# Optimization experiments

Measured on AMD Instinct MI355X. Metric: run time of the kernel, lower is better.

Reference implementation:

```python
import math
import jax, jax.numpy as jnp
import numpy as np

B, S, D, H, KV = 2, 2048, 1024, 16, 4
HD = D // H  # 64
ROPE_BASE = 10000.0
RMS_EPS = 1.1920929e-07  # torch.finfo(float32).eps, F.rms_norm default


def setup_inputs() -> dict:
    key = jax.random.key(0)
    ks = jax.random.split(key, 5)
    x = jax.random.normal(ks[0], (B, S, D), jnp.float32)
    Wq = jax.random.normal(ks[1], (D, D), jnp.float32) * 0.02
    Wk = jax.random.normal(ks[2], (KV * HD, D), jnp.float32) * 0.02
    Wv = jax.random.normal(ks[3], (KV * HD, D), jnp.float32) * 0.02
    Wproj = jax.random.normal(ks[4], (D, D), jnp.float32) * 0.02
    q_gain = jnp.ones((H,), jnp.float32)  # qk_gain_init = 1.0
    return {"x": x, "Wq": Wq, "Wk": Wk, "Wv": Wv, "Wproj": Wproj, "q_gain": q_gain}


def _rms_norm(t):
    # F.rms_norm with no weight: t * rsqrt(mean(t^2) + eps)
    return t * jax.lax.rsqrt(jnp.mean(t * t, axis=-1, keepdims=True) + RMS_EPS)


def _rope(t, cos, sin):
    half = t.shape[-1] // 2
    t1, t2 = t[..., :half], t[..., half:]
    return jnp.concatenate([t1 * cos + t2 * sin, t1 * -sin + t2 * cos], axis=-1)


def reference(x, Wq, Wk, Wv, Wproj, q_gain):
    bsz, seqlen, dim = x.shape
    hd = dim // H
    # QKV projections (Linear weight layout [out, in])
    q = (x @ Wq.T).reshape(bsz, seqlen, H, hd).transpose(0, 2, 1, 3)    # [B,H,S,hd]
    k = (x @ Wk.T).reshape(bsz, seqlen, KV, hd).transpose(0, 2, 1, 3)   # [B,KV,S,hd]
    v = (x @ Wv.T).reshape(bsz, seqlen, KV, hd).transpose(0, 2, 1, 3)
    # per-head RMSNorm on q/k (no learned weight)
    q = _rms_norm(q)
    k = _rms_norm(k)
    # RoPE tables
    inv_freq = 1.0 / (ROPE_BASE ** (jnp.arange(0, hd, 2, dtype=jnp.float32) / hd))
    t = jnp.arange(seqlen, dtype=jnp.float32)
    freqs = t[:, None] * inv_freq[None, :]                              # [S, hd/2]
    cos = jnp.cos(freqs)[None, None]                                    # [1,1,S,hd/2]
    sin = jnp.sin(freqs)[None, None]
    q = _rope(q, cos, sin)
    k = _rope(k, cos, sin)
    # learned per-head query gain
    q = q * q_gain[None, :, None, None]
    # GQA: repeat_interleave kv heads to full head count
    rep = H // KV
    k = jnp.repeat(k, rep, axis=1)                                      # [B,H,S,hd]
    v = jnp.repeat(v, rep, axis=1)
    # causal SDPA, scale = 1/sqrt(head_dim)
    scores = jnp.einsum("bhqd,bhkd->bhqk", q, k) * (1.0 / math.sqrt(hd))
    causal = jnp.tril(jnp.ones((seqlen, seqlen), bool))
    scores = jnp.where(causal[None, None], scores, jnp.finfo(scores.dtype).min)
    attn = jax.nn.softmax(scores, axis=-1)
    y = jnp.einsum("bhqk,bhkd->bhqd", attn, v)
    y = y.transpose(0, 2, 1, 3).reshape(bsz, seqlen, dim)
    return y @ Wproj.T
```

## Files before the change

### kernel.cpp

```cpp
#include <hip/hip_runtime.h>

typedef unsigned short u16;
typedef __bf16 bf16_t;
typedef bf16_t bf16x8 __attribute__((ext_vector_type(8)));
typedef float f32x4 __attribute__((ext_vector_type(4)));
typedef u16 u16x8 __attribute__((ext_vector_type(8)));
typedef u16 u16x4 __attribute__((ext_vector_type(4)));

__device__ __forceinline__ u16 f2bf(float f) {
  unsigned u = __float_as_uint(f);
  u += 0x7fffu + ((u >> 16) & 1u);
  return (u16)(u >> 16);
}

__device__ __forceinline__ float bf2f(u16 u) {
  return __uint_as_float((unsigned)u << 16);
}

__device__ __forceinline__ unsigned cvtpk(float lo, float hi) {
  unsigned r;
  asm("v_cvt_pk_bf16_f32 %0, %1, %2" : "=v"(r) : "v"(lo), "v"(hi));
  return r;
}

__device__ __forceinline__ f32x4 mfma16(bf16x8 a, bf16x8 b, f32x4 c) {
  return __builtin_amdgcn_mfma_f32_16x16x32_bf16(a, b, c, 0, 0, 0);
}

__device__ __forceinline__ void gl2lds16(const u16* g, u16* l) {
  __builtin_amdgcn_global_load_lds(
      (__attribute__((address_space(1))) void*)(u16*)g,
      (__attribute__((address_space(3))) void*)l, 16, 0, 0);
}

__device__ __forceinline__ void cast8(const float* __restrict__ in,
                                      u16* __restrict__ out, int i) {
  float4 a = *(const float4*)&in[i];
  float4 b = *(const float4*)&in[i + 4];
  uint4 o;
  o.x = cvtpk(a.x, a.y);
  o.y = cvtpk(a.z, a.w);
  o.z = cvtpk(b.x, b.y);
  o.w = cvtpk(b.z, b.w);
  *(uint4*)&out[i] = o;
}

__global__ __launch_bounds__(256) void megacast(
    const float* __restrict__ x, const float* __restrict__ Wq,
    const float* __restrict__ Wk, const float* __restrict__ Wv,
    const float* __restrict__ Wp, u16* __restrict__ xb,
    u16* __restrict__ wallb, u16* __restrict__ wpb,
    float2* __restrict__ tbl) {
  const int blk = blockIdx.x;
  const int tid = threadIdx.x;
  if (blk < 2048) {
    cast8(x, xb, (blk * 256 + tid) * 8);
  } else if (blk < 2560) {
    cast8(Wq, wallb, ((blk - 2048) * 256 + tid) * 8);
  } else if (blk < 2688) {
    cast8(Wk, wallb + 1048576, ((blk - 2560) * 256 + tid) * 8);
  } else if (blk < 2816) {
    cast8(Wv, wallb + 1310720, ((blk - 2688) * 256 + tid) * 8);
  } else if (blk < 3328) {
    cast8(Wp, wpb, ((blk - 2816) * 256 + tid) * 8);
  } else {
    const int idx = (blk - 3328) * 256 + tid;
    const int s = idx >> 5, i = idx & 31;
    float inv = exp2f(-(float)i * (13.287712379549449f / 32.0f));
    float fr = (float)s * inv;
    float sn, cs;
    sincosf(fr, &sn, &cs);
    tbl[idx] = make_float2(cs, sn);
  }
}

template <int BM, int BN, bool O16>
__global__ __launch_bounds__(256) void gemm_bt(const u16* __restrict__ A,
                                               const u16* __restrict__ B,
                                               void* __restrict__ Cv,
                                               int M, int N, int K) {
  constexpr int FM = BM / 32;
  constexpr int FN = BN / 32;
  constexpr int NL = (BM + BN) / 32;
  __shared__ __align__(16) u16 As[2][BM][64];
  __shared__ __align__(16) u16 Bs[2][BN][64];
  const int tid = threadIdx.x;
  const int lane = tid & 63;
  const int lg = lane >> 4, li = lane & 15;
  const int wave = tid >> 6;
  const int wr = (wave >> 1) * (BM / 2), wc = (wave & 1) * (BN / 2);
  const int m0 = blockIdx.y * BM, n0 = blockIdx.x * BN;

  const int s_r = tid >> 3;
  const int s_c = (tid & 7) ^ ((tid >> 3) & 7);
  const int rdsw = li & 7;

  auto GSTAGE = [&](int buf, int k0) {
    const u16* ga = &A[(size_t)(m0 + s_r) * K + k0 + s_c * 8];
#pragma unroll
    for (int i = 0; i < BM / 32; i++)
      gl2lds16(ga + (size_t)(i * 32) * K, &As[buf][i * 32][0] + (size_t)tid * 8);
    const u16* gb = &B[(size_t)(n0 + s_r) * K + k0 + s_c * 8];
#pragma unroll
    for (int i = 0; i < BN / 32; i++)
      gl2lds16(gb + (size_t)(i * 32) * K, &Bs[buf][i * 32][0] + (size_t)tid * 8);
  };

  const f32x4 fz = {0.f, 0.f, 0.f, 0.f};
  f32x4 acc[FM][FN];
#pragma unroll
  for (int i = 0; i < FM; i++)
#pragma unroll
    for (int j = 0; j < FN; j++) acc[i][j] = fz;

  GSTAGE(0, 0);
  int buf = 0;
  const int nk = K >> 6;
  for (int t = 0; t < nk; ++t) {
    if (t + 1 < nk) {
      GSTAGE(buf ^ 1, (t + 1) * 64);
      if constexpr (NL == 6)
        asm volatile("s_waitcnt vmcnt(6)" ::: "memory");
      else if constexpr (NL == 7)
        asm volatile("s_waitcnt vmcnt(7)" ::: "memory");
      else
        asm volatile("s_waitcnt vmcnt(8)" ::: "memory");
    } else {
      asm volatile("s_waitcnt vmcnt(0)" ::: "memory");
    }
    __builtin_amdgcn_s_barrier();
#pragma unroll
    for (int kk = 0; kk < 2; kk++) {
      bf16x8 af[FM], bfr[FN];
#pragma unroll
      for (int i = 0; i < FM; i++)
        af[i] = *(const bf16x8*)&As[buf][wr + i * 16 + li]
                                   [((kk * 4 + lg) ^ rdsw) * 8];
#pragma unroll
      for (int j = 0; j < FN; j++)
        bfr[j] = *(const bf16x8*)&Bs[buf][wc + j * 16 + li]
                                    [((kk * 4 + lg) ^ rdsw) * 8];
      __builtin_amdgcn_s_setprio(1);
#pragma unroll
      for (int i = 0; i < FM; i++)
#pragma unroll
        for (int j = 0; j < FN; j++) acc[i][j] = mfma16(af[i], bfr[j], acc[i][j]);
      __builtin_amdgcn_s_setprio(0);
    }
    __builtin_amdgcn_s_barrier();
    buf ^= 1;
  }
#pragma unroll
  for (int i = 0; i < FM; i++)
#pragma unroll
    for (int j = 0; j < FN; j++)
#pragma unroll
      for (int r = 0; r < 4; r++) {
        const size_t idx =
            (size_t)(m0 + wr + i * 16 + lg * 4 + r) * N + n0 + wc + j * 16 + li;
        if constexpr (O16)
          ((u16*)Cv)[idx] = f2bf(acc[i][j][r]);
        else
          ((float*)Cv)[idx] = acc[i][j][r];
      }
}

__global__ __launch_bounds__(256) void rmsropeqk(const u16* __restrict__ in,
                                                 const float* __restrict__ qg,
                                                 u16* __restrict__ qhb,
                                                 u16* __restrict__ khb, int S,
                                                 const float2* __restrict__ tbl) {
  const int w = threadIdx.x >> 6;
  const int t = threadIdx.x & 63;
  const int row = blockIdx.x * 4 + w;
  const int h = blockIdx.y;
  const bool isq = h < 16;
  const int col = isq ? h * 64 : 1024 + (h - 16) * 64;
  const float v = bf2f(in[(size_t)row * 1536 + col + t]);
  float ss = v * v;
#pragma unroll
  for (int m = 1; m < 64; m <<= 1) ss += __shfl_xor(ss, m);
  const float vn = v * rsqrtf(ss * (1.0f / 64.0f) + 1.1920929e-07f);
  const float partner = __shfl_xor(vn, 32);
  const int b = row / S;
  const int s = row - b * S;
  const float2 cs2 = tbl[s * 32 + (t & 31)];
  float o = (t < 32) ? (vn * cs2.x + partner * cs2.y)
                     : (vn * cs2.x - partner * cs2.y);
  if (isq) {
    o *= 0.18033688011112042f * qg[h];
    qhb[((size_t)(b * 16 + h) * S + s) * 64 + t] = f2bf(o);
  } else {
    khb[((size_t)(b * 4 + (h - 16)) * S + s) * 64 + t] = f2bf(o);
  }
}

__global__ __launch_bounds__(256) void vcast2(const u16* __restrict__ qf,
                                              u16* __restrict__ vt, int S) {
  const int blk = blockIdx.x;
  const int sc = blk & 7;
  const int kv = (blk >> 3) & 3;
  const int b = blk >> 5;
  __shared__ u16 T[256][66];
  const int tid = threadIdx.x;
  const int dcol = tid & 63;
  const int w = tid >> 6;
  const u16* src =
      qf + (size_t)(b * S + sc * 256) * 1536 + 1280 + kv * 64 + dcol;
#pragma unroll 4
  for (int i = 0; i < 64; ++i) {
    const int sl = i * 4 + w;
    T[sl][dcol] = src[(size_t)sl * 1536];
  }
  __syncthreads();
  u16* dst = vt + (size_t)((b * 4 + kv) * 64) * S + sc * 256;
  const int l = tid & 63;
#pragma unroll 4
  for (int i = 0; i < 16; ++i) {
    const int drow = i * 4 + w;
    u16x4 v4;
    v4[0] = T[l * 4 + 0][drow];
    v4[1] = T[l * 4 + 1][drow];
    v4[2] = T[l * 4 + 2][drow];
    v4[3] = T[l * 4 + 3][drow];
    *(u16x4*)(dst + (size_t)drow * S + l * 4) = v4;
  }
}

__global__ __launch_bounds__(256) void attn8(const u16* __restrict__ qh,
                                             const u16* __restrict__ kh,
                                             const u16* __restrict__ vt,
                                             const float* __restrict__ qg,
                                             u16* __restrict__ y, int S) {
  const int bh = blockIdx.x & 31;
  const int g = blockIdx.x >> 5;
  const int d = g & 7, u = g >> 3;
  const int qb = (u == 0) ? 31 - d : (u == 1) ? 16 + d : (u == 2) ? 15 - d : d;
  const int h = bh & 15, b = bh >> 4;
  const int kvh = h >> 2;
  const int tid = threadIdx.x;
  const int wave = tid >> 6;
  const int lane = tid & 63;
  const int lg = lane >> 4, li = lane & 15;
  const int q0 = qb * 64 + wave * 16;
  const int qrow = q0 + li;
  const float mrow = 11.541560327111707f * fabsf(qg[h]);

  const u16* qp = qh + ((size_t)(b * 16 + h) * S + q0) * 64;
  const u16* kp = kh + (size_t)(b * 4 + kvh) * S * 64;
  const u16* vp = vt + (size_t)(b * 4 + kvh) * 64 * S;

  __shared__ __align__(16) u16 Ks[2][64][64];
  __shared__ __align__(16) u16 Vs[2][64][64];
  __shared__ __align__(16) u16 Ps[4][16][64];

  const int s_r0 = tid >> 3;
  const int s_c = (tid & 7) ^ ((tid >> 3) & 7);
  char* psrow = (char*)&Ps[wave][li][0];
  const int swz = li & 7;
  const int rdsw = li & 7;
  const f32x4 minit = {-mrow, -mrow, -mrow, -mrow};
  const f32x4 fz = {0.f, 0.f, 0.f, 0.f};
  const u16x8 ones_u = {0x3F80, 0x3F80, 0x3F80, 0x3F80,
                        0x3F80, 0x3F80, 0x3F80, 0x3F80};
  const bf16x8 onesb = *(const bf16x8*)&ones_u;

#define STAGE(buf, kb)                                                        \
  {                                                                           \
    const u16* gk = kp + (size_t)((kb) + s_r0) * 64 + s_c * 8;                \
    gl2lds16(gk, &Ks[buf][0][0] + (size_t)tid * 8);                           \
    gl2lds16(gk + (size_t)32 * 64, &Ks[buf][32][0] + (size_t)tid * 8);        \
    const u16* gv = vp + (size_t)s_r0 * S + (kb) + s_c * 8;                   \
    gl2lds16(gv, &Vs[buf][0][0] + (size_t)tid * 8);                           \
    gl2lds16(gv + (size_t)32 * S, &Vs[buf][32][0] + (size_t)tid * 8);         \
  }

  STAGE(0, 0)
  const bf16x8 qf0 = *(const bf16x8*)&qp[li * 64 + lg * 8];
  const bf16x8 qf1 = *(const bf16x8*)&qp[li * 64 + 32 + lg * 8];

  f32x4 o[4];
#pragma unroll
  for (int j = 0; j < 4; j++) o[j] = fz;
  f32x4 lsum = fz;

  int buf = 0;
  for (int tt = 0; tt <= qb; ++tt) {
    if (tt < qb) {
      STAGE(buf ^ 1, (tt + 1) * 64)
      asm volatile("s_waitcnt vmcnt(4)" ::: "memory");
    } else {
      asm volatile("s_waitcnt vmcnt(0)" ::: "memory");
    }
    __builtin_amdgcn_s_barrier();
    const int kb = tt * 64;
    f32x4 s[4];
    __builtin_amdgcn_s_setprio(1);
#pragma unroll
    for (int t = 0; t < 4; t++) {
      const bf16x8 ka =
          *(const bf16x8*)&Ks[buf][t * 16 + li][((lg) ^ rdsw) * 8];
      const bf16x8 kc =
          *(const bf16x8*)&Ks[buf][t * 16 + li][((lg + 4) ^ rdsw) * 8];
      s[t] = mfma16(ka, qf0, minit);
      s[t] = mfma16(kc, qf1, s[t]);
    }
    __builtin_amdgcn_s_setprio(0);
    float pv[16];
    if (tt < qb) {
#pragma unroll
      for (int t = 0; t < 4; t++)
#pragma unroll
        for (int r = 0; r < 4; r++) pv[t * 4 + r] = exp2f(s[t][r]);
    } else {
#pragma unroll
      for (int t = 0; t < 4; t++)
#pragma unroll
        for (int r = 0; r < 4; r++) {
          const float x =
              (kb + t * 16 + lg * 4 + r > qrow) ? -1e30f : s[t][r];
          pv[t * 4 + r] = exp2f(x);
        }
    }
#pragma unroll
    for (int t = 0; t < 4; t++) {
      uint2 w;
      w.x = cvtpk(pv[t * 4 + 0], pv[t * 4 + 1]);
      w.y = cvtpk(pv[t * 4 + 2], pv[t * 4 + 3]);
      const int c8 = (t * 4 + lg) ^ (swz << 1);
      *(uint2*)(psrow + c8 * 8) = w;
    }
    const bf16x8 pa0 = *(const bf16x8*)(psrow + ((lg + 0) ^ swz) * 16);
    const bf16x8 pa1 = *(const bf16x8*)(psrow + ((lg + 4) ^ swz) * 16);
    __builtin_amdgcn_s_setprio(1);
#pragma unroll
    for (int j = 0; j < 4; j++) {
      const bf16x8 v0 =
          *(const bf16x8*)&Vs[buf][j * 16 + li][((lg) ^ rdsw) * 8];
      const bf16x8 v1 =
          *(const bf16x8*)&Vs[buf][j * 16 + li][((lg + 4) ^ rdsw) * 8];
      o[j] = mfma16(pa0, v0, o[j]);
      o[j] = mfma16(pa1, v1, o[j]);
    }
    lsum = mfma16(pa0, onesb, lsum);
    lsum = mfma16(pa1, onesb, lsum);
    __builtin_amdgcn_s_setprio(0);
    __builtin_amdgcn_s_barrier();
    buf ^= 1;
  }
#undef STAGE
#pragma unroll
  for (int j = 0; j < 4; j++)
#pragma unroll
    for (int r = 0; r < 4; r++)
      y[((size_t)(b * S + q0 + lg * 4 + r)) * 1024 + h * 64 + j * 16 + li] =
          f2bf(o[j][r] / lsum[r]);
}

extern "C" void kernel_launch(void* const* d_in, const int* in_sizes, int n_in,
                              void* d_out, int out_size, void* d_ws, size_t ws_size,
                              hipStream_t stream) {
  const float* x  = (const float*)d_in[0];
  const float* Wq = (const float*)d_in[1];
  const float* Wk = (const float*)d_in[2];
  const float* Wv = (const float*)d_in[3];
  const float* Wp = (const float*)d_in[4];
  const float* qg = (const float*)d_in[5];
  float* out = (float*)d_out;

  const int S = 2048;
  char* ws = (char*)d_ws;
  u16*    xb    = (u16*)(ws + 0);
  u16*    wallb = (u16*)(ws + 8388608);
  u16*    wpb   = (u16*)(ws + 11534336);
  float2* tbl   = (float2*)(ws + 13631488);
  u16*    qf    = (u16*)(ws + 14155776);
  u16*    qhb   = (u16*)(ws + 26738688);
  u16*    khb   = (u16*)(ws + 35127296);
  u16*    vtb   = (u16*)(ws + 37224448);
  u16*    yb    = (u16*)(ws + 39321600);
  if (ws_size < 47710208) return;

  megacast<<<3584, 256, 0, stream>>>(x, Wq, Wk, Wv, Wp, xb, wallb, wpb, tbl);

  gemm_bt<128, 96, true><<<dim3(16, 32), 256, 0, stream>>>(xb, wallb, qf,
                                                           4096, 1536, 1024);

  rmsropeqk<<<dim3(1024, 20), 256, 0, stream>>>(qf, qg, qhb, khb, S, tbl);
  vcast2<<<64, 256, 0, stream>>>(qf, vtb, S);

  attn8<<<1024, 256, 0, stream>>>(qhb, khb, vtb, qg, yb, S);

  gemm_bt<64, 128, false><<<dim3(8, 64), 256, 0, stream>>>(yb, wpb, out,
                                                           4096, 1024, 1024);
}
```

Measured before the change: 107.0 us.

## Split long causal query tiles across two blocks with partial-sum reduction

Replaces the attention kernel's per-block query-tile assignment with a balanced split. Long query tiles (31-dd) are processed in two halves by separate blocks, and one of those blocks also handles the short tile dd. Every block therefore does roughly 16-17 KV iterations. Partial O and row sums go to fp32 scratch that reuses dead workspace regions (xb and qf), and a new reduction kernel combines them and writes bf16 output. This removes tail imbalance from causal work but adds scratch traffic and an extra launch. No max subtraction is needed because a fixed bound is used.

```diff
diff --git a/kernel.cpp b/kernel.cpp
--- a/kernel.cpp
+++ b/kernel.cpp
@@ -227,26 +227,26 @@
   }
 }
 
-__global__ __launch_bounds__(256) void attn8(const u16* __restrict__ qh,
+__global__ __launch_bounds__(256) void attn9(const u16* __restrict__ qh,
                                              const u16* __restrict__ kh,
                                              const u16* __restrict__ vt,
                                              const float* __restrict__ qg,
-                                             u16* __restrict__ y, int S) {
-  const int bh = blockIdx.x & 31;
-  const int g = blockIdx.x >> 5;
-  const int d = g & 7, u = g >> 3;
-  const int qb = (u == 0) ? 31 - d : (u == 1) ? 16 + d : (u == 2) ? 15 - d : d;
+                                             u16* __restrict__ y,
+                                             float* __restrict__ scr0,
+                                             float* __restrict__ scr1, int S) {
+  const int idx = blockIdx.x;
+  const int half = idx & 1;
+  const int dd = (idx >> 1) & 15;
+  const int bh = idx >> 5;
   const int h = bh & 15, b = bh >> 4;
   const int kvh = h >> 2;
+  const int p = bh * 16 + dd;
   const int tid = threadIdx.x;
   const int wave = tid >> 6;
   const int lane = tid & 63;
   const int lg = lane >> 4, li = lane & 15;
-  const int q0 = qb * 64 + wave * 16;
-  const int qrow = q0 + li;
   const float mrow = 11.541560327111707f * fabsf(qg[h]);
 
-  const u16* qp = qh + ((size_t)(b * 16 + h) * S + q0) * 64;
   const u16* kp = kh + (size_t)(b * 4 + kvh) * S * 64;
   const u16* vp = vt + (size_t)(b * 4 + kvh) * 64 * S;
 
@@ -275,86 +275,144 @@
     gl2lds16(gv + (size_t)32 * S, &Vs[buf][32][0] + (size_t)tid * 8);         \
   }
 
-  STAGE(0, 0)
-  const bf16x8 qf0 = *(const bf16x8*)&qp[li * 64 + lg * 8];
-  const bf16x8 qf1 = *(const bf16x8*)&qp[li * 64 + 32 + lg * 8];
-
-  f32x4 o[4];
-#pragma unroll
-  for (int j = 0; j < 4; j++) o[j] = fz;
-  f32x4 lsum = fz;
-
   int buf = 0;
-  for (int tt = 0; tt <= qb; ++tt) {
-    if (tt < qb) {
-      STAGE(buf ^ 1, (tt + 1) * 64)
-      asm volatile("s_waitcnt vmcnt(4)" ::: "memory");
+
+  auto runseg = [&](int qt, int t0, int t1, int mode, int next_t0) {
+    const int q0 = qt * 64 + wave * 16;
+    const int qrow = q0 + li;
+    const u16* qp = qh + ((size_t)(b * 16 + h) * S + q0) * 64;
+    const bf16x8 qf0 = *(const bf16x8*)&qp[li * 64 + lg * 8];
+    const bf16x8 qf1 = *(const bf16x8*)&qp[li * 64 + 32 + lg * 8];
+    f32x4 o[4];
+#pragma unroll
+    for (int j = 0; j < 4; j++) o[j] = fz;
+    f32x4 lsum = fz;
+
+    for (int tt = t0; tt < t1; ++tt) {
+      if (tt + 1 < t1) {
+        STAGE(buf ^ 1, (tt + 1) * 64)
+        asm volatile("s_waitcnt vmcnt(4)" ::: "memory");
+      } else if (next_t0 >= 0) {
+        STAGE(buf ^ 1, next_t0 * 64)
+        asm volatile("s_waitcnt vmcnt(4)" ::: "memory");
+      } else {
+        asm volatile("s_waitcnt vmcnt(0)" ::: "memory");
+      }
+      __builtin_amdgcn_s_barrier();
+      const int kb = tt * 64;
+      f32x4 s[4];
+      __builtin_amdgcn_s_setprio(1);
+#pragma unroll
+      for (int t = 0; t < 4; t++) {
+        const bf16x8 ka =
+            *(const bf16x8*)&Ks[buf][t * 16 + li][((lg) ^ rdsw) * 8];
+        const bf16x8 kc =
+            *(const bf16x8*)&Ks[buf][t * 16 + li][((lg + 4) ^ rdsw) * 8];
+        s[t] = mfma16(ka, qf0, minit);
+        s[t] = mfma16(kc, qf1, s[t]);
+      }
+      __builtin_amdgcn_s_setprio(0);
+      float pv[16];
+      if (tt == qt) {
+#pragma unroll
+        for (int t = 0; t < 4; t++)
+#pragma unroll
+          for (int r = 0; r < 4; r++) {
+            const float x =
+                (kb + t * 16 + lg * 4 + r > qrow) ? -1e30f : s[t][r];
+            pv[t * 4 + r] = exp2f(x);
+          }
+      } else {
+#pragma unroll
+        for (int t = 0; t < 4; t++)
+#pragma unroll
+          for (int r = 0; r < 4; r++) pv[t * 4 + r] = exp2f(s[t][r]);
+      }
+#pragma unroll
+      for (int t = 0; t < 4; t++) {
+        uint2 w;
+        w.x = cvtpk(pv[t * 4 + 0], pv[t * 4 + 1]);
+        w.y = cvtpk(pv[t * 4 + 2], pv[t * 4 + 3]);
+        const int c8 = (t * 4 + lg) ^ (swz << 1);
+        *(uint2*)(psrow + c8 * 8) = w;
+      }
+      const bf16x8 pa0 = *(const bf16x8*)(psrow + ((lg + 0) ^ swz) * 16);
+      const bf16x8 pa1 = *(const bf16x8*)(psrow + ((lg + 4) ^ swz) * 16);
+      __builtin_amdgcn_s_setprio(1);
+#pragma unroll
+      for (int j = 0; j < 4; j++) {
+        const bf16x8 v0 =
+            *(const bf16x8*)&Vs[buf][j * 16 + li][((lg) ^ rdsw) * 8];
+        const bf16x8 v1 =
+            *(const bf16x8*)&Vs[buf][j * 16 + li][((lg + 4) ^ rdsw) * 8];
+        o[j] = mfma16(pa0, v0, o[j]);
+        o[j] = mfma16(pa1, v1, o[j]);
+      }
+      lsum = mfma16(pa0, onesb, lsum);
+      lsum = mfma16(pa1, onesb, lsum);
+      __builtin_amdgcn_s_setprio(0);
+      __builtin_amdgcn_s_barrier();
+      buf ^= 1;
+    }
+
+    if (mode == 2) {
+#pragma unroll
+      for (int j = 0; j < 4; j++)
+#pragma unroll
+        for (int r = 0; r < 4; r++)
+          y[((size_t)(b * S + q0 + lg * 4 + r)) * 1024 + h * 64 + j * 16 + li] =
+              f2bf(o[j][r] / lsum[r]);
     } else {
-      asm volatile("s_waitcnt vmcnt(0)" ::: "memory");
+      float* scr = (mode == 0 ? scr0 : scr1) + (size_t)p * 4160;
+#pragma unroll
+      for (int j = 0; j < 4; j++)
+#pragma unroll
+        for (int r = 0; r < 4; r++)
+          scr[(wave * 16 + lg * 4 + r) * 64 + j * 16 + li] = o[j][r];
+      if (li == 0) {
+#pragma unroll
+        for (int r = 0; r < 4; r++)
+          scr[4096 + wave * 16 + lg * 4 + r] = lsum[r];
+      }
     }
-    __builtin_amdgcn_s_barrier();
-    const int kb = tt * 64;
-    f32x4 s[4];
-    __builtin_amdgcn_s_setprio(1);
-#pragma unroll
-    for (int t = 0; t < 4; t++) {
-      const bf16x8 ka =
-          *(const bf16x8*)&Ks[buf][t * 16 + li][((lg) ^ rdsw) * 8];
-      const bf16x8 kc =
-          *(const bf16x8*)&Ks[buf][t * 16 + li][((lg + 4) ^ rdsw) * 8];
-      s[t] = mfma16(ka, qf0, minit);
-      s[t] = mfma16(kc, qf1, s[t]);
-    }
-    __builtin_amdgcn_s_setprio(0);
-    float pv[16];
-    if (tt < qb) {
-#pragma unroll
-      for (int t = 0; t < 4; t++)
-#pragma unroll
-        for (int r = 0; r < 4; r++) pv[t * 4 + r] = exp2f(s[t][r]);
-    } else {
-#pragma unroll
-      for (int t = 0; t < 4; t++)
-#pragma unroll
-        for (int r = 0; r < 4; r++) {
-          const float x =
-              (kb + t * 16 + lg * 4 + r > qrow) ? -1e30f : s[t][r];
-          pv[t * 4 + r] = exp2f(x);
-        }
-    }
-#pragma unroll
-    for (int t = 0; t < 4; t++) {
-      uint2 w;
-      w.x = cvtpk(pv[t * 4 + 0], pv[t * 4 + 1]);
-      w.y = cvtpk(pv[t * 4 + 2], pv[t * 4 + 3]);
-      const int c8 = (t * 4 + lg) ^ (swz << 1);
-      *(uint2*)(psrow + c8 * 8) = w;
-    }
-    const bf16x8 pa0 = *(const bf16x8*)(psrow + ((lg + 0) ^ swz) * 16);
-    const bf16x8 pa1 = *(const bf16x8*)(psrow + ((lg + 4) ^ swz) * 16);
-    __builtin_amdgcn_s_setprio(1);
-#pragma unroll
-    for (int j = 0; j < 4; j++) {
-      const bf16x8 v0 =
-          *(const bf16x8*)&Vs[buf][j * 16 + li][((lg) ^ rdsw) * 8];
-      const bf16x8 v1 =
-          *(const bf16x8*)&Vs[buf][j * 16 + li][((lg + 4) ^ rdsw) * 8];
-      o[j] = mfma16(pa0, v0, o[j]);
-      o[j] = mfma16(pa1, v1, o[j]);
-    }
-    lsum = mfma16(pa0, onesb, lsum);
-    lsum = mfma16(pa1, onesb, lsum);
-    __builtin_amdgcn_s_setprio(0);
-    __builtin_amdgcn_s_barrier();
-    buf ^= 1;
+  };
+
+  if (half == 0) {
+    STAGE(0, 0)
+    runseg(31 - dd, 0, 16, 0, -1);
+  } else {
+    STAGE(0, 16 * 64)
+    runseg(31 - dd, 16, 32 - dd, 1, 0);
+    runseg(dd, 0, dd + 1, 2, -1);
   }
 #undef STAGE
-#pragma unroll
-  for (int j = 0; j < 4; j++)
-#pragma unroll
-    for (int r = 0; r < 4; r++)
-      y[((size_t)(b * S + q0 + lg * 4 + r)) * 1024 + h * 64 + j * 16 + li] =
-          f2bf(o[j][r] / lsum[r]);
+}
+
+__global__ __launch_bounds__(256) void attnred(const float* __restrict__ scr0,
+                                               const float* __restrict__ scr1,
+                                               u16* __restrict__ y, int S) {
+  const int p = blockIdx.x;
+  const int bh = p >> 4, dd = p & 15;
+  const int qt = 31 - dd;
+  const int b = bh >> 4, h = bh & 15;
+  const int tid = threadIdx.x;
+  const int row = tid >> 2, cq = (tid & 3) * 16;
+  const size_t base = (size_t)p * 4160;
+  const float linv =
+      1.0f / (scr0[base + 4096 + row] + scr1[base + 4096 + row]);
+  const float* o0 = scr0 + base + row * 64 + cq;
+  const float* o1 = scr1 + base + row * 64 + cq;
+  u16 ov[16];
+#pragma unroll
+  for (int c = 0; c < 16; c += 4) {
+    float4 a = *(const float4*)(o0 + c);
+    float4 bb = *(const float4*)(o1 + c);
+    *(unsigned*)&ov[c] = cvtpk((a.x + bb.x) * linv, (a.y + bb.y) * linv);
+    *(unsigned*)&ov[c + 2] = cvtpk((a.z + bb.z) * linv, (a.w + bb.w) * linv);
+  }
+  u16* yp = &y[((size_t)(b * S + qt * 64 + row)) * 1024 + h * 64 + cq];
+  *(uint4*)yp = *(uint4*)&ov[0];
+  *(uint4*)(yp + 8) = *(uint4*)&ov[8];
 }
 
 extern "C" void kernel_launch(void* const* d_in, const int* in_sizes, int n_in,
@@ -379,6 +437,8 @@
   u16*    khb   = (u16*)(ws + 35127296);
   u16*    vtb   = (u16*)(ws + 37224448);
   u16*    yb    = (u16*)(ws + 39321600);
+  float*  scr0  = (float*)(ws + 0);
+  float*  scr1  = (float*)(ws + 14155776);
   if (ws_size < 47710208) return;
 
   megacast<<<3584, 256, 0, stream>>>(x, Wq, Wk, Wv, Wp, xb, wallb, wpb, tbl);
@@ -389,7 +449,8 @@
   rmsropeqk<<<dim3(1024, 20), 256, 0, stream>>>(qf, qg, qhb, khb, S, tbl);
   vcast2<<<64, 256, 0, stream>>>(qf, vtb, S);
 
-  attn8<<<1024, 256, 0, stream>>>(qhb, khb, vtb, qg, yb, S);
+  attn9<<<1024, 256, 0, stream>>>(qhb, khb, vtb, qg, yb, scr0, scr1, S);
+  attnred<<<512, 256, 0, stream>>>(scr0, scr1, yb, S);
 
   gemm_bt<64, 128, false><<<dim3(8, 64), 256, 0, stream>>>(yb, wpb, out,
                                                            4096, 1024, 1024);
```

Result: slower. 117.9 us (+10.2%).

## Process 128 query rows per attention block to reuse K/V tiles

Applied to the files above, without the earlier changes.

The attention kernel now gives each wave 32 query rows (two 16-row groups) instead of 16, so each block covers 128 queries and half as many blocks are launched. Each K/V tile staged into shared memory and each K/V fragment read from it now feeds twice as many MFMAs, which cuts global and LDS traffic per unit of work. The cost is higher register pressure (launch bounds now ask for two blocks per CU), fewer blocks to balance the causal workload, and extra masked work on diagonal tiles because of the coarser query granularity.

```diff
diff --git a/kernel.cpp b/kernel.cpp
--- a/kernel.cpp
+++ b/kernel.cpp
@@ -227,36 +227,35 @@
   }
 }
 
-__global__ __launch_bounds__(256) void attn8(const u16* __restrict__ qh,
-                                             const u16* __restrict__ kh,
-                                             const u16* __restrict__ vt,
-                                             const float* __restrict__ qg,
-                                             u16* __restrict__ y, int S) {
-  const int bh = blockIdx.x & 31;
-  const int g = blockIdx.x >> 5;
-  const int d = g & 7, u = g >> 3;
-  const int qb = (u == 0) ? 31 - d : (u == 1) ? 16 + d : (u == 2) ? 15 - d : d;
+__global__ __launch_bounds__(256, 2) void attn10(const u16* __restrict__ qh,
+                                                 const u16* __restrict__ kh,
+                                                 const u16* __restrict__ vt,
+                                                 const float* __restrict__ qg,
+                                                 u16* __restrict__ y, int S) {
+  const int i = blockIdx.x;
+  const int bh = i & 31;
+  const int t = (i < 256) ? 15 - (i >> 5) : (i >> 5) - 8;
   const int h = bh & 15, b = bh >> 4;
   const int kvh = h >> 2;
   const int tid = threadIdx.x;
   const int wave = tid >> 6;
   const int lane = tid & 63;
   const int lg = lane >> 4, li = lane & 15;
-  const int q0 = qb * 64 + wave * 16;
-  const int qrow = q0 + li;
+  const int q0w = t * 128 + wave * 32;
   const float mrow = 11.541560327111707f * fabsf(qg[h]);
 
-  const u16* qp = qh + ((size_t)(b * 16 + h) * S + q0) * 64;
+  const u16* qp = qh + ((size_t)(b * 16 + h) * S + q0w) * 64;
   const u16* kp = kh + (size_t)(b * 4 + kvh) * S * 64;
   const u16* vp = vt + (size_t)(b * 4 + kvh) * 64 * S;
 
   __shared__ __align__(16) u16 Ks[2][64][64];
   __shared__ __align__(16) u16 Vs[2][64][64];
-  __shared__ __align__(16) u16 Ps[4][16][64];
+  __shared__ __align__(16) u16 Ps[4][32][64];
 
   const int s_r0 = tid >> 3;
   const int s_c = (tid & 7) ^ ((tid >> 3) & 7);
-  char* psrow = (char*)&Ps[wave][li][0];
+  char* psrow0 = (char*)&Ps[wave][li][0];
+  char* psrow1 = (char*)&Ps[wave][16 + li][0];
   const int swz = li & 7;
   const int rdsw = li & 7;
   const f32x4 minit = {-mrow, -mrow, -mrow, -mrow};
@@ -276,17 +275,24 @@
   }
 
   STAGE(0, 0)
-  const bf16x8 qf0 = *(const bf16x8*)&qp[li * 64 + lg * 8];
-  const bf16x8 qf1 = *(const bf16x8*)&qp[li * 64 + 32 + lg * 8];
-
-  f32x4 o[4];
-#pragma unroll
-  for (int j = 0; j < 4; j++) o[j] = fz;
-  f32x4 lsum = fz;
-
+  bf16x8 qf0[2], qf1[2];
+#pragma unroll
+  for (int g = 0; g < 2; g++) {
+    qf0[g] = *(const bf16x8*)&qp[(g * 16 + li) * 64 + lg * 8];
+    qf1[g] = *(const bf16x8*)&qp[(g * 16 + li) * 64 + 32 + lg * 8];
+  }
+
+  f32x4 o[4][2];
+#pragma unroll
+  for (int j = 0; j < 4; j++)
+#pragma unroll
+    for (int g = 0; g < 2; g++) o[j][g] = fz;
+  f32x4 lsum[2] = {fz, fz};
+
+  const int nkv = 2 * t + 2;
   int buf = 0;
-  for (int tt = 0; tt <= qb; ++tt) {
-    if (tt < qb) {
+  for (int tt = 0; tt < nkv; ++tt) {
+    if (tt + 1 < nkv) {
       STAGE(buf ^ 1, (tt + 1) * 64)
       asm volatile("s_waitcnt vmcnt(4)" ::: "memory");
     } else {
@@ -294,44 +300,58 @@
     }
     __builtin_amdgcn_s_barrier();
     const int kb = tt * 64;
-    f32x4 s[4];
+    f32x4 s[4][2];
     __builtin_amdgcn_s_setprio(1);
 #pragma unroll
-    for (int t = 0; t < 4; t++) {
+    for (int t4 = 0; t4 < 4; t4++) {
       const bf16x8 ka =
-          *(const bf16x8*)&Ks[buf][t * 16 + li][((lg) ^ rdsw) * 8];
+          *(const bf16x8*)&Ks[buf][t4 * 16 + li][((lg) ^ rdsw) * 8];
       const bf16x8 kc =
-          *(const bf16x8*)&Ks[buf][t * 16 + li][((lg + 4) ^ rdsw) * 8];
-      s[t] = mfma16(ka, qf0, minit);
-      s[t] = mfma16(kc, qf1, s[t]);
+          *(const bf16x8*)&Ks[buf][t4 * 16 + li][((lg + 4) ^ rdsw) * 8];
+#pragma unroll
+      for (int g = 0; g < 2; g++) {
+        s[t4][g] = mfma16(ka, qf0[g], minit);
+        s[t4][g] = mfma16(kc, qf1[g], s[t4][g]);
+      }
     }
     __builtin_amdgcn_s_setprio(0);
-    float pv[16];
-    if (tt < qb) {
-#pragma unroll
-      for (int t = 0; t < 4; t++)
-#pragma unroll
-        for (int r = 0; r < 4; r++) pv[t * 4 + r] = exp2f(s[t][r]);
+    float pv[2][16];
+    if (kb + 63 <= q0w) {
+#pragma unroll
+      for (int t4 = 0; t4 < 4; t4++)
+#pragma unroll
+        for (int g = 0; g < 2; g++)
+#pragma unroll
+          for (int r = 0; r < 4; r++)
+            pv[g][t4 * 4 + r] = exp2f(s[t4][g][r]);
     } else {
 #pragma unroll
-      for (int t = 0; t < 4; t++)
-#pragma unroll
-        for (int r = 0; r < 4; r++) {
-          const float x =
-              (kb + t * 16 + lg * 4 + r > qrow) ? -1e30f : s[t][r];
-          pv[t * 4 + r] = exp2f(x);
-        }
-    }
-#pragma unroll
-    for (int t = 0; t < 4; t++) {
-      uint2 w;
-      w.x = cvtpk(pv[t * 4 + 0], pv[t * 4 + 1]);
-      w.y = cvtpk(pv[t * 4 + 2], pv[t * 4 + 3]);
-      const int c8 = (t * 4 + lg) ^ (swz << 1);
-      *(uint2*)(psrow + c8 * 8) = w;
-    }
-    const bf16x8 pa0 = *(const bf16x8*)(psrow + ((lg + 0) ^ swz) * 16);
-    const bf16x8 pa1 = *(const bf16x8*)(psrow + ((lg + 4) ^ swz) * 16);
+      for (int t4 = 0; t4 < 4; t4++)
+#pragma unroll
+        for (int g = 0; g < 2; g++)
+#pragma unroll
+          for (int r = 0; r < 4; r++) {
+            const int key = kb + t4 * 16 + lg * 4 + r;
+            const int qrow = q0w + g * 16 + li;
+            pv[g][t4 * 4 + r] = exp2f(key > qrow ? -1e30f : s[t4][g][r]);
+          }
+    }
+#pragma unroll
+    for (int t4 = 0; t4 < 4; t4++) {
+      const int c8 = (t4 * 4 + lg) ^ (swz << 1);
+      uint2 w0, w1;
+      w0.x = cvtpk(pv[0][t4 * 4 + 0], pv[0][t4 * 4 + 1]);
+      w0.y = cvtpk(pv[0][t4 * 4 + 2], pv[0][t4 * 4 + 3]);
+      w1.x = cvtpk(pv[1][t4 * 4 + 0], pv[1][t4 * 4 + 1]);
+      w1.y = cvtpk(pv[1][t4 * 4 + 2], pv[1][t4 * 4 + 3]);
+      *(uint2*)(psrow0 + c8 * 8) = w0;
+      *(uint2*)(psrow1 + c8 * 8) = w1;
+    }
+    bf16x8 pa0[2], pa1[2];
+    pa0[0] = *(const bf16x8*)(psrow0 + ((lg + 0) ^ swz) * 16);
+    pa1[0] = *(const bf16x8*)(psrow0 + ((lg + 4) ^ swz) * 16);
+    pa0[1] = *(const bf16x8*)(psrow1 + ((lg + 0) ^ swz) * 16);
+    pa1[1] = *(const bf16x8*)(psrow1 + ((lg + 4) ^ swz) * 16);
     __builtin_amdgcn_s_setprio(1);
 #pragma unroll
     for (int j = 0; j < 4; j++) {
@@ -339,22 +359,30 @@
           *(const bf16x8*)&Vs[buf][j * 16 + li][((lg) ^ rdsw) * 8];
       const bf16x8 v1 =
           *(const bf16x8*)&Vs[buf][j * 16 + li][((lg + 4) ^ rdsw) * 8];
-      o[j] = mfma16(pa0, v0, o[j]);
-      o[j] = mfma16(pa1, v1, o[j]);
-    }
-    lsum = mfma16(pa0, onesb, lsum);
-    lsum = mfma16(pa1, onesb, lsum);
+#pragma unroll
+      for (int g = 0; g < 2; g++) {
+        o[j][g] = mfma16(pa0[g], v0, o[j][g]);
+        o[j][g] = mfma16(pa1[g], v1, o[j][g]);
+      }
+    }
+#pragma unroll
+    for (int g = 0; g < 2; g++) {
+      lsum[g] = mfma16(pa0[g], onesb, lsum[g]);
+      lsum[g] = mfma16(pa1[g], onesb, lsum[g]);
+    }
     __builtin_amdgcn_s_setprio(0);
     __builtin_amdgcn_s_barrier();
     buf ^= 1;
   }
 #undef STAGE
 #pragma unroll
-  for (int j = 0; j < 4; j++)
-#pragma unroll
-    for (int r = 0; r < 4; r++)
-      y[((size_t)(b * S + q0 + lg * 4 + r)) * 1024 + h * 64 + j * 16 + li] =
-          f2bf(o[j][r] / lsum[r]);
+  for (int g = 0; g < 2; g++)
+#pragma unroll
+    for (int j = 0; j < 4; j++)
+#pragma unroll
+      for (int r = 0; r < 4; r++)
+        y[((size_t)(b * S + q0w + g * 16 + lg * 4 + r)) * 1024 + h * 64 +
+          j * 16 + li] = f2bf(o[j][g][r] / lsum[g][r]);
 }
 
 extern "C" void kernel_launch(void* const* d_in, const int* in_sizes, int n_in,
@@ -389,7 +417,7 @@
   rmsropeqk<<<dim3(1024, 20), 256, 0, stream>>>(qf, qg, qhb, khb, S, tbl);
   vcast2<<<64, 256, 0, stream>>>(qf, vtb, S);
 
-  attn8<<<1024, 256, 0, stream>>>(qhb, khb, vtb, qg, yb, S);
+  attn10<<<512, 256, 0, stream>>>(qhb, khb, vtb, qg, yb, S);
 
   gemm_bt<64, 128, false><<<dim3(8, 64), 256, 0, stream>>>(yb, wpb, out,
                                                            4096, 1024, 1024);
```

New measurement: 116.7 us. 1.09x slower.
